# Kernel optimization log

Measured on AMD Instinct MI355X. Metric: run time of the kernel, lower is better.

The kernel has to match this reference:

```python
import jax, jax.numpy as jnp
import numpy as np

B, T, V, D, H, DK = 64, 384, 12, 256, 4, 64

def _ln(x, g, b):
    m = jnp.mean(x, -1, keepdims=True)
    v = jnp.var(x, -1, keepdims=True)
    return (x - m) * jax.lax.rsqrt(v + 1e-5) * g + b

def _grn(x, W1, b1, W2, b2, Wg, bg, lng, lnb, ctx=None, Wc=None, Ws=None, bs=None):
    # eta2 = ELU(fc1(x) + ctx_proj(ctx)); eta1 = fc2(eta2); GLU; residual; LN
    h = x @ W1 + b1
    if ctx is not None:
        h = h + ctx @ Wc
    h = jax.nn.elu(h)
    h = h @ W2 + b2
    g = h @ Wg + bg
    a, gate = jnp.split(g, 2, axis=-1)
    gated = a * jax.nn.sigmoid(gate)
    skip = x if Ws is None else x @ Ws + bs
    return _ln(skip + gated, lng, lnb)

def setup_inputs() -> dict:
    key = jax.random.key(0)
    ks = iter(jax.random.split(key, 48))
    def rn(shape, s=0.02):
        return jax.random.normal(next(ks), shape, jnp.float32) * s
    return {
        'x': jax.random.normal(next(ks), (B, T, V, D), jnp.float32),
        'context': jax.random.normal(next(ks), (B, D), jnp.float32),
        # flattened GRN of VSN: in=V*D, hidden=D, out=V, context=D, skip needed
        'fg_W1': rn((V * D, D)), 'fg_b1': jnp.zeros((D,), jnp.float32),
        'fg_Wc': rn((D, D)),
        'fg_W2': rn((D, D)), 'fg_b2': jnp.zeros((D,), jnp.float32),
        'fg_Wg': rn((D, 2 * V)), 'fg_bg': jnp.zeros((2 * V,), jnp.float32),
        'fg_Ws': rn((V * D, V)), 'fg_bs': jnp.zeros((V,), jnp.float32),
        'fg_lng': jnp.ones((V,), jnp.float32), 'fg_lnb': jnp.zeros((V,), jnp.float32),
        # per-variable GRNs (V of them, in=out=hidden=D, no skip/ctx), stacked
        'sv_W1': rn((V, D, D)), 'sv_b1': jnp.zeros((V, D), jnp.float32),
        'sv_W2': rn((V, D, D)), 'sv_b2': jnp.zeros((V, D), jnp.float32),
        'sv_Wg': rn((V, D, 2 * D)), 'sv_bg': jnp.zeros((V, 2 * D), jnp.float32),
        'sv_lng': jnp.ones((V, D), jnp.float32), 'sv_lnb': jnp.zeros((V, D), jnp.float32),
        # static enrichment GRN: in=out=hidden=D with context
        'en_W1': rn((D, D)), 'en_b1': jnp.zeros((D,), jnp.float32),
        'en_Wc': rn((D, D)),
        'en_W2': rn((D, D)), 'en_b2': jnp.zeros((D,), jnp.float32),
        'en_Wg': rn((D, 2 * D)), 'en_bg': jnp.zeros((2 * D,), jnp.float32),
        'en_lng': jnp.ones((D,), jnp.float32), 'en_lnb': jnp.zeros((D,), jnp.float32),
        # interpretable MHA: per-head Q/K, shared V, output proj
        'Wq': rn((H, D, DK)), 'Wk': rn((H, D, DK)),
        'Wv': rn((D, DK)), 'Wo': rn((DK, D)),
    }

def reference(x, context, fg_W1, fg_b1, fg_Wc, fg_W2, fg_b2, fg_Wg, fg_bg, fg_Ws, fg_bs,
              fg_lng, fg_lnb, sv_W1, sv_b1, sv_W2, sv_b2, sv_Wg, sv_bg, sv_lng, sv_lnb,
              en_W1, en_b1, en_Wc, en_W2, en_b2, en_Wg, en_bg, en_lng, en_lnb,
              Wq, Wk, Wv, Wo):
    b, t, v, d = x.shape
    ctx3 = context[:, None, :]  # broadcast static context over time
    # ---- Variable Selection Network ----
    xf = x.reshape(b, t, v * d)
    w = _grn(xf, fg_W1, fg_b1, fg_W2, fg_b2, fg_Wg, fg_bg, fg_lng, fg_lnb,
             ctx=ctx3, Wc=fg_Wc, Ws=fg_Ws, bs=fg_bs)
    w = jax.nn.softmax(w, axis=-1)  # (b,t,v)
    per_var = jax.vmap(_grn, in_axes=(2, 0, 0, 0, 0, 0, 0, 0, 0), out_axes=2)(
        x, sv_W1, sv_b1, sv_W2, sv_b2, sv_Wg, sv_bg, sv_lng, sv_lnb)  # (b,t,v,d)
    sel = jnp.sum(per_var * w[..., None], axis=2)  # (b,t,d)
    # ---- static enrichment GRN ----
    enr = _grn(sel, en_W1, en_b1, en_W2, en_b2, en_Wg, en_bg, en_lng, en_lnb,
               ctx=ctx3, Wc=en_Wc)
    # ---- interpretable multi-head attention (causal), per-head Q/K, shared V ----
    q = jnp.einsum('btd,hdk->hbtk', enr, Wq)
    k = jnp.einsum('btd,hdk->hbtk', enr, Wk)
    vp = enr @ Wv  # (b,t,dk), shared across heads
    scale = jax.lax.rsqrt(jnp.asarray(DK, jnp.float32))
    scores = jnp.einsum('hbqd,hbkd->hbqk', q, k) * scale
    mask = jnp.triu(jnp.ones((t, t), bool), 1)  # True = masked (future)
    scores = jnp.where(mask, jnp.asarray(-1e9, scores.dtype), scores)
    attn = jax.nn.softmax(scores, axis=-1)
    heads = jnp.einsum('hbqk,bkd->hbqd', attn, vp)
    out = jnp.mean(heads, axis=0) @ Wo  # mean over heads then shared output proj
    return out
```

## Files before the change

kernel.cpp:

```cpp
#include <hip/hip_runtime.h>
#include <hip/hip_bf16.h>
#include <stdint.h>
#include <stddef.h>

typedef __bf16 bf16;
typedef __bf16 bf16x8 __attribute__((ext_vector_type(8)));
typedef float  f32x4  __attribute__((ext_vector_type(4)));

#define BTR 24576
#define EPI_BIAS  1
#define EPI_CVEC  2
#define EPI_ELU   4
#define EPI_ATTN  8
#define EPI_GATE  32
#define EPI_PERM  64

typedef const __attribute__((address_space(1))) void gas_void;
typedef __attribute__((address_space(3))) void sas_void;
__device__ __forceinline__ void gload16(const void* g, void* s) {
  __builtin_amdgcn_global_load_lds((gas_void*)g, (sas_void*)s, 16, 0, 0);
}

__device__ __forceinline__ int perm512(int n) {
  return (n < 256) ? (((n >> 4) << 5) + (n & 15))
                   : ((((n - 256) >> 4) << 5) + ((n - 256) & 15) + 16);
}

template<int EPI, bool AF32, bool CF32>
__global__ __launch_bounds__(256, 2)
void gemm_kernel(const void* __restrict__ Av, int lda, long sAh, long sAb,
                 const bf16* __restrict__ Bt, int ldb, long sBh, long sBb,
                 void* __restrict__ Cv, int ldc, long sC,
                 int K, int zdiv,
                 const float* __restrict__ bias, const float* __restrict__ cvec,
                 long sBias)
{
  __shared__ __align__(16) bf16 As[2][128 * 32];
  __shared__ __align__(16) bf16 Bs[2][128 * 32];

  const int tid  = threadIdx.x;
  const int wave = tid >> 6, lane = tid & 63;
  const int wr = wave >> 1, wc = wave & 1;
  const int quad = lane >> 4, l16 = lane & 15;

  const int z  = blockIdx.z;
  const int hh = z / zdiv, bb = z % zdiv;
  const float* AbF = nullptr; const bf16* AbH = nullptr;
  if constexpr (AF32) AbF = (const float*)Av + (long)hh * sAh + (long)bb * sAb;
  else                AbH = (const bf16*)Av  + (long)hh * sAh + (long)bb * sAb;
  const bf16* Bb = Bt + (long)hh * sBh + (long)bb * sBb;
  float* CbF = nullptr; bf16* CbH = nullptr;
  if constexpr (CF32) CbF = (float*)Cv + (long)z * sC;
  else                CbH = (bf16*)Cv  + (long)z * sC;

  const int rowBase = blockIdx.y * 128;
  const int colBase = blockIdx.x * 128;

  f32x4 acc[4][4];
#pragma unroll
  for (int i = 0; i < 4; ++i)
#pragma unroll
    for (int j = 0; j < 4; ++j) { acc[i][j][0]=0.f; acc[i][j][1]=0.f; acc[i][j][2]=0.f; acc[i][j][3]=0.f; }

  const int r0 = tid >> 2, kc = tid & 3;
  const int r1 = tid >> 1, kh = (tid & 1) * 16;
  const int arow = (wr * 64 + l16) * 32 + quad * 8;
  const int brow = (wc * 64 + l16) * 32 + quad * 8;

  char* AsW = (char*)&As[0][0] + wave * 1024;
  char* BsW = (char*)&Bs[0][0] + wave * 1024;

  f32x4 pf0, pf1, pf2, pf3;
  const int nt = K >> 5;
  int cur = 0;

  if constexpr (AF32) {
    const float* p = AbF + (size_t)(rowBase + r1) * lda + kh;
    pf0 = *(const f32x4*)(p);     pf1 = *(const f32x4*)(p + 4);
    pf2 = *(const f32x4*)(p + 8); pf3 = *(const f32x4*)(p + 12);
  } else {
    gload16(AbH + (size_t)(rowBase + r0)      * lda + kc * 8, AsW);
    gload16(AbH + (size_t)(rowBase + 64 + r0) * lda + kc * 8, AsW + 4096);
  }
  gload16(Bb + (size_t)(colBase + r0)      * ldb + kc * 8, BsW);
  gload16(Bb + (size_t)(colBase + 64 + r0) * ldb + kc * 8, BsW + 4096);
  if constexpr (AF32) {
    bf16x8 a0, a1;
#pragma unroll
    for (int e = 0; e < 4; ++e) {
      a0[e] = (bf16)pf0[e]; a0[4 + e] = (bf16)pf1[e];
      a1[e] = (bf16)pf2[e]; a1[4 + e] = (bf16)pf3[e];
    }
    *(bf16x8*)(&As[0][0] + r1 * 32 + kh)     = a0;
    *(bf16x8*)(&As[0][0] + r1 * 32 + kh + 8) = a1;
  }
  __syncthreads();

  for (int t = 0; t < nt; ++t) {
    const int nxt = cur ^ 1;
    if (t + 1 < nt) {
      const int k1 = (t + 1) * 32;
      if constexpr (AF32) {
        const float* p = AbF + (size_t)(rowBase + r1) * lda + k1 + kh;
        pf0 = *(const f32x4*)(p);     pf1 = *(const f32x4*)(p + 4);
        pf2 = *(const f32x4*)(p + 8); pf3 = *(const f32x4*)(p + 12);
      } else {
        gload16(AbH + (size_t)(rowBase + r0)      * lda + k1 + kc * 8, AsW + nxt * 8192);
        gload16(AbH + (size_t)(rowBase + 64 + r0) * lda + k1 + kc * 8, AsW + nxt * 8192 + 4096);
      }
      gload16(Bb + (size_t)(colBase + r0)      * ldb + k1 + kc * 8, BsW + nxt * 8192);
      gload16(Bb + (size_t)(colBase + 64 + r0) * ldb + k1 + kc * 8, BsW + nxt * 8192 + 4096);
    }

    const bf16* Asc = &As[cur][0];
    const bf16* Bsc = &Bs[cur][0];
    bf16x8 af[4], bfv[4];
#pragma unroll
    for (int mi = 0; mi < 4; ++mi) af[mi]  = *(const bf16x8*)(Asc + arow + mi * 512);
#pragma unroll
    for (int ni = 0; ni < 4; ++ni) bfv[ni] = *(const bf16x8*)(Bsc + brow + ni * 512);
#pragma unroll
    for (int mi = 0; mi < 4; ++mi)
#pragma unroll
      for (int ni = 0; ni < 4; ++ni)
        acc[mi][ni] = __builtin_amdgcn_mfma_f32_16x16x32_bf16(af[mi], bfv[ni], acc[mi][ni], 0, 0, 0);

    if constexpr (AF32) {
      if (t + 1 < nt) {
        bf16x8 a0, a1;
#pragma unroll
        for (int e = 0; e < 4; ++e) {
          a0[e] = (bf16)pf0[e]; a0[4 + e] = (bf16)pf1[e];
          a1[e] = (bf16)pf2[e]; a1[4 + e] = (bf16)pf3[e];
        }
        *(bf16x8*)(&As[nxt][0] + r1 * 32 + kh)     = a0;
        *(bf16x8*)(&As[nxt][0] + r1 * 32 + kh + 8) = a1;
      }
    }
    __syncthreads();
    cur = nxt;
  }

  if constexpr (EPI & EPI_GATE) {
    const float* bp = bias + (size_t)z * sBias;
#pragma unroll
    for (int mi = 0; mi < 4; ++mi) {
#pragma unroll
      for (int nj = 0; nj < 2; ++nj) {
        const int ni = nj * 2;
        const int pa = colBase + wc * 64 + ni * 16 + l16;
        const int j  = (colBase >> 1) + wc * 32 + nj * 16 + l16;
        const float ba = bp[pa], bg = bp[pa + 16];
        const int row0 = rowBase + wr * 64 + mi * 16 + quad * 4;
#pragma unroll
        for (int r = 0; r < 4; ++r) {
          float a = acc[mi][ni][r]     + ba;
          float g = acc[mi][ni + 1][r] + bg;
          CbH[(size_t)(row0 + r) * ldc + j] = (bf16)(a / (1.f + __expf(-g)));
        }
      }
    }
    return;
  }
  const int bctx = (EPI & EPI_CVEC) ? (rowBase / 384) : 0;
  const float* bp = (EPI & EPI_BIAS) ? bias + (size_t)z * sBias : nullptr;
#pragma unroll
  for (int mi = 0; mi < 4; ++mi) {
#pragma unroll
    for (int ni = 0; ni < 4; ++ni) {
      const int row0 = rowBase + wr * 64 + mi * 16 + quad * 4;
      const int col  = colBase + wc * 64 + ni * 16 + l16;
      float bv = (EPI & EPI_BIAS) ? bp[col] : 0.f;
      float cv = (EPI & EPI_CVEC) ? cvec[bctx * 256 + col] : 0.f;
#pragma unroll
      for (int r = 0; r < 4; ++r) {
        float v = acc[mi][ni][r] + bv + cv;
        if (EPI & EPI_ELU)  v = v > 0.f ? v : __expf(v) - 1.f;
        if (EPI & EPI_ATTN) { v *= 0.125f; if (col > row0 + r) v = -1e9f; }
        int srow = row0 + r;
        if constexpr (EPI & EPI_PERM) srow = perm512(srow);
        if constexpr (CF32) CbF[(size_t)srow * ldc + col] = v;
        else                CbH[(size_t)srow * ldc + col] = (bf16)v;
      }
    }
  }
}

__global__ __launch_bounds__(256, 2)
void fgwide_kernel(const float* __restrict__ A, const bf16* __restrict__ Bt,
                   bf16* __restrict__ C, const float* __restrict__ bias,
                   const float* __restrict__ cvec)
{
  __shared__ __align__(16) bf16 As[2][64 * 32];
  __shared__ __align__(16) bf16 Bs[2][384 * 32];
  const int tid = threadIdx.x;
  const int wave = tid >> 6, lane = tid & 63;
  const int quad = lane >> 4, l16 = lane & 15;
  const int rowBase = blockIdx.x * 64;

  f32x4 acc[4][6];
#pragma unroll
  for (int i = 0; i < 4; ++i)
#pragma unroll
    for (int j = 0; j < 6; ++j) { acc[i][j][0]=0.f; acc[i][j][1]=0.f; acc[i][j][2]=0.f; acc[i][j][3]=0.f; }

  const int r1 = tid >> 2, kh = (tid & 3) * 8;
  const int arow = l16 * 32 + quad * 8;
  const int brow = (wave * 96 + l16) * 32 + quad * 8;

  char* BsW = (char*)&Bs[0][0] + wave * 1024;

  f32x4 pf0, pf1;
  int cur = 0;

  {
    const float* p = A + (size_t)(rowBase + r1) * 3072 + kh;
    pf0 = *(const f32x4*)(p); pf1 = *(const f32x4*)(p + 4);
#pragma unroll
    for (int c = 0; c < 6; ++c) {
      const int idx = c * 256 + tid, rb = idx >> 2, kc2 = idx & 3;
      gload16(Bt + (size_t)rb * 3072 + kc2 * 8, BsW + c * 4096);
    }
    bf16x8 av;
#pragma unroll
    for (int e = 0; e < 4; ++e) { av[e] = (bf16)pf0[e]; av[4 + e] = (bf16)pf1[e]; }
    *(bf16x8*)(&As[0][0] + r1 * 32 + kh) = av;
  }
  __syncthreads();

  for (int t = 0; t < 96; ++t) {
    const int nxt = cur ^ 1;
    if (t + 1 < 96) {
      const int k1 = (t + 1) * 32;
      const float* p = A + (size_t)(rowBase + r1) * 3072 + k1 + kh;
      pf0 = *(const f32x4*)(p); pf1 = *(const f32x4*)(p + 4);
#pragma unroll
      for (int c = 0; c < 6; ++c) {
        const int idx = c * 256 + tid, rb = idx >> 2, kc2 = idx & 3;
        gload16(Bt + (size_t)rb * 3072 + k1 + kc2 * 8, BsW + nxt * 24576 + c * 4096);
      }
    }

    const bf16* Asc = &As[cur][0];
    const bf16* Bsc = &Bs[cur][0];
    bf16x8 af[4], bfv[6];
#pragma unroll
    for (int mi = 0; mi < 4; ++mi) af[mi]  = *(const bf16x8*)(Asc + arow + mi * 512);
#pragma unroll
    for (int ni = 0; ni < 6; ++ni) bfv[ni] = *(const bf16x8*)(Bsc + brow + ni * 512);
#pragma unroll
    for (int mi = 0; mi < 4; ++mi)
#pragma unroll
      for (int ni = 0; ni < 6; ++ni)
        acc[mi][ni] = __builtin_amdgcn_mfma_f32_16x16x32_bf16(af[mi], bfv[ni], acc[mi][ni], 0, 0, 0);

    if (t + 1 < 96) {
      bf16x8 av;
#pragma unroll
      for (int e = 0; e < 4; ++e) { av[e] = (bf16)pf0[e]; av[4 + e] = (bf16)pf1[e]; }
      *(bf16x8*)(&As[nxt][0] + r1 * 32 + kh) = av;
    }
    __syncthreads();
    cur = nxt;
  }

  const int bctx = rowBase / 384;
#pragma unroll
  for (int mi = 0; mi < 4; ++mi) {
#pragma unroll
    for (int ni = 0; ni < 6; ++ni) {
      const int col = wave * 96 + ni * 16 + l16;
      const bool act = (wave * 96 + ni * 16) < 256;
      const float bv = bias[col];
      const float cv = act ? cvec[bctx * 256 + col] : 0.f;
      const int row0 = rowBase + mi * 16 + quad * 4;
#pragma unroll
      for (int r = 0; r < 4; ++r) {
        float v = acc[mi][ni][r] + bv + cv;
        if (act) v = v > 0.f ? v : __expf(v) - 1.f;
        C[(size_t)(row0 + r) * 384 + col] = (bf16)v;
      }
    }
  }
}

__global__ void prep_kernel(
    const float* fgW1, const float* fgWs, const float* fgW2, const float* fgWg,
    const float* fgb1, const float* fgbs,
    const float* svW1, const float* svWg, const float* svW2,
    const float* enW1, const float* enWg, const float* enW2,
    const float* Wq, const float* Wk, const float* Wv, const float* Wo,
    bf16* fgW1WsT, bf16* fgWgPT, bf16* fgW2C, float* bias384,
    bf16* svW1T, bf16* svWgT, bf16* svW2C,
    bf16* enW1T, bf16* enWgT, bf16* enW2C,
    bf16* WqkvT, bf16* WoT)
{
  long i = (long)blockIdx.x * 256 + threadIdx.x;
  if (i < 1179648) {
    int n = i / 3072, k = i % 3072; float v;
    if (n < 256) v = fgW1[(size_t)k * 256 + n];
    else { int nn = n - 256; v = (nn < 12) ? fgWs[(size_t)k * 12 + nn] : 0.f; }
    fgW1WsT[i] = (bf16)v; return; } i -= 1179648;
  if (i < 32768)  { int n = i >> 8, k = i & 255; fgWgPT[i] = (n < 24) ? (bf16)fgWg[k * 24 + n] : (bf16)0.f; return; } i -= 32768;
  if (i < 65536)  { fgW2C[i] = (bf16)fgW2[i]; return; } i -= 65536;
  if (i < 384)    { bias384[i] = (i < 256) ? fgb1[i] : ((i < 268) ? fgbs[i - 256] : 0.f); return; } i -= 384;
  if (i < 786432) { long v = i >> 16, r = i & 65535; int n = r >> 8, k = r & 255; svW1T[i] = (bf16)svW1[(v << 16) + k * 256 + n]; return; } i -= 786432;
  if (i < 1572864){ long v = i >> 17, r = i & 131071; int n = r >> 8, k = r & 255; svWgT[i] = (bf16)svWg[(v << 17) + k * 512 + n]; return; } i -= 1572864;
  if (i < 786432) { svW2C[i] = (bf16)svW2[i]; return; } i -= 786432;
  if (i < 65536)  { int n = i >> 8, k = i & 255; enW1T[i] = (bf16)enW1[k * 256 + n]; return; } i -= 65536;
  if (i < 131072) { int n = i >> 8, k = i & 255; enWgT[i] = (bf16)enWg[k * 512 + n]; return; } i -= 131072;
  if (i < 65536)  { enW2C[i] = (bf16)enW2[i]; return; } i -= 65536;
  if (i < 163840) { int n = i >> 8, k = i & 255; float val;
                    if (n < 256)      val = Wq[(n >> 6) * 16384 + k * 64 + (n & 63)];
                    else if (n < 512) { int nn = n - 256; val = Wk[(nn >> 6) * 16384 + k * 64 + (nn & 63)]; }
                    else if (n < 576) val = Wv[k * 64 + (n - 512)];
                    else              val = 0.f;
                    WqkvT[i] = (bf16)val; return; } i -= 163840;
  if (i < 16384)  { int n = i >> 6, k = i & 63; WoT[i] = (bf16)Wo[k * 256 + n]; }
}

__global__ void biasfuse_kernel(const float* fgb2, const float* fgWg, const float* fgbg,
                                const float* svb2, const float* svWg, const float* svbg,
                                const float* enb2, const float* enWg, const float* enbg,
                                float* fgBF, float* svBFP, float* enBFP)
{
  int i = blockIdx.x * 256 + threadIdx.x;
  if (i < 128) {
    float s = 0.f;
    if (i < 24) { s = fgbg[i]; for (int k = 0; k < 256; ++k) s += fgb2[k] * fgWg[k * 24 + i]; }
    fgBF[i] = s; return; } i -= 128;
  if (i < 6144) {
    int v = i >> 9, n = i & 511;
    float s = svbg[v * 512 + n];
    const float* W = svWg + (size_t)v * 131072;
    const float* b2 = svb2 + v * 256;
    for (int k = 0; k < 256; ++k) s += b2[k] * W[k * 512 + n];
    svBFP[v * 512 + perm512(n)] = s; return; } i -= 6144;
  if (i < 512) {
    float s = enbg[i];
    for (int k = 0; k < 256; ++k) s += enb2[k] * enWg[k * 512 + i];
    enBFP[perm512(i)] = s; }
}

__global__ void cvec_kernel(const float* __restrict__ ctx, const float* __restrict__ WcFg,
                            const float* __restrict__ WcEn, float* __restrict__ outFg,
                            float* __restrict__ outEn) {
  int b = blockIdx.x, n = threadIdx.x;
  const float* Wc = blockIdx.y ? WcEn : WcFg;
  float* o = blockIdx.y ? outEn : outFg;
  float acc = 0.f;
  for (int d = 0; d < 256; ++d) acc += ctx[b * 256 + d] * Wc[d * 256 + n];
  o[b * 256 + n] = acc;
}

__global__ void lnsm12_kernel(const bf16* __restrict__ B384, const bf16* __restrict__ GP,
                              const float* __restrict__ lng, const float* __restrict__ lnb,
                              float* __restrict__ w) {
  int r = blockIdx.x * 256 + threadIdx.x;
  if (r >= BTR) return;
  float y[12]; float m = 0.f;
#pragma unroll
  for (int j = 0; j < 12; ++j) {
    float a = (float)GP[(size_t)r * 128 + j];
    float g = (float)GP[(size_t)r * 128 + 12 + j];
    float gated = a / (1.f + __expf(-g));
    y[j] = (float)B384[(size_t)r * 384 + 256 + j] + gated; m += y[j];
  }
  m *= (1.f / 12.f);
  float var = 0.f;
#pragma unroll
  for (int j = 0; j < 12; ++j) { float d = y[j] - m; var += d * d; }
  var *= (1.f / 12.f);
  float rstd = rsqrtf(var + 1e-5f);
  float mx = -1e30f;
#pragma unroll
  for (int j = 0; j < 12; ++j) { y[j] = (y[j] - m) * rstd * lng[j] + lnb[j]; mx = fmaxf(mx, y[j]); }
  float s = 0.f;
#pragma unroll
  for (int j = 0; j < 12; ++j) { y[j] = __expf(y[j] - mx); s += y[j]; }
  float inv = 1.f / s;
#pragma unroll
  for (int j = 0; j < 12; ++j) w[r * 12 + j] = y[j] * inv;
}

__device__ __forceinline__ void block_sum2(float a, float b, float& oa, float& ob) {
#pragma unroll
  for (int o = 32; o; o >>= 1) { a += __shfl_xor(a, o); b += __shfl_xor(b, o); }
  __shared__ float ra[4], rb[4];
  int w = threadIdx.x >> 6;
  if ((threadIdx.x & 63) == 0) { ra[w] = a; rb[w] = b; }
  __syncthreads();
  oa = ra[0] + ra[1] + ra[2] + ra[3];
  ob = rb[0] + rb[1] + rb[2] + rb[3];
  __syncthreads();
}

__global__ __launch_bounds__(256)
void selacc4_kernel(const bf16* __restrict__ GATED, const float* __restrict__ x,
                    const float* __restrict__ w, const float* __restrict__ lng,
                    const float* __restrict__ lnb, float* __restrict__ sel,
                    bf16* __restrict__ selb, int v0, int isFirst, int isLast) {
  int r = blockIdx.x, d = threadIdx.x;
  float acc = isFirst ? 0.f : sel[(size_t)r * 256 + d];
#pragma unroll
  for (int vv = 0; vv < 4; ++vv) {
    int v = v0 + vv;
    float gated = (float)GATED[(size_t)vv * ((size_t)BTR * 256) + (size_t)r * 256 + d];
    float y = x[(size_t)r * 3072 + v * 256 + d] + gated;
    float s1, s2;
    block_sum2(y, y * y, s1, s2);
    float mean = s1 * (1.f / 256.f);
    float var  = s2 * (1.f / 256.f) - mean * mean;
    float val  = (y - mean) * rsqrtf(var + 1e-5f) * lng[v * 256 + d] + lnb[v * 256 + d];
    acc += w[r * 12 + v] * val;
  }
  if (isLast) selb[(size_t)r * 256 + d] = (bf16)acc;
  else        sel[(size_t)r * 256 + d] = acc;
}

__global__ __launch_bounds__(256)
void enrln_kernel(const bf16* __restrict__ GATED, const bf16* __restrict__ skip,
                  const float* __restrict__ lng, const float* __restrict__ lnb,
                  bf16* __restrict__ out) {
  int r = blockIdx.x, d = threadIdx.x;
  float gated = (float)GATED[(size_t)r * 256 + d];
  float y = (float)skip[(size_t)r * 256 + d] + gated;
  float s1, s2;
  block_sum2(y, y * y, s1, s2);
  float mean = s1 * (1.f / 256.f);
  float var = s2 * (1.f / 256.f) - mean * mean;
  float norm = (y - mean) * rsqrtf(var + 1e-5f);
  out[(size_t)r * 256 + d] = (bf16)(norm * lng[d] + lnb[d]);
}

__global__ __launch_bounds__(384)
void softmax_avg_kernel(const bf16* __restrict__ S, bf16* __restrict__ P) {
  const int bq = blockIdx.x;
  const int b = bq / 384, q = bq % 384;
  const int j = threadIdx.x;
  const int w = j >> 6;
  __shared__ float red[6];
  float pb = 0.f;
  for (int h = 0; h < 4; ++h) {
    float s = (float)S[((size_t)((h * 64 + b) * 384 + q)) * 384 + j];
    float m = s;
#pragma unroll
    for (int o = 32; o; o >>= 1) m = fmaxf(m, __shfl_xor(m, o));
    if ((j & 63) == 0) red[w] = m;
    __syncthreads();
    m = fmaxf(fmaxf(fmaxf(red[0], red[1]), fmaxf(red[2], red[3])), fmaxf(red[4], red[5]));
    __syncthreads();
    float e = __expf(s - m);
    float l = e;
#pragma unroll
    for (int o = 32; o; o >>= 1) l += __shfl_xor(l, o);
    if ((j & 63) == 0) red[w] = l;
    __syncthreads();
    l = red[0] + red[1] + red[2] + red[3] + red[4] + red[5];
    __syncthreads();
    pb += e / l;
  }
  P[(size_t)bq * 384 + j] = (bf16)(0.25f * pb);
}

template<int EPI, bool AF32, bool CF32>
static inline void rungemm(hipStream_t s,
    const void* A, int lda, const bf16* Bt, int ldb, void* C, int ldc,
    int M, int N, int K,
    const float* bias = nullptr, const float* cvec = nullptr,
    int Z = 1, int zdiv = 1,
    long sAh = 0, long sAb = 0, long sBh = 0, long sBb = 0, long sC = 0, long sBias = 0)
{
  dim3 grid(N / 128, M / 128, Z);
  gemm_kernel<EPI, AF32, CF32><<<grid, 256, 0, s>>>(A, lda, sAh, sAb, Bt, ldb, sBh, sBb, C, ldc, sC, K, zdiv, bias, cvec, sBias);
}

extern "C" void kernel_launch(void* const* d_in, const int* in_sizes, int n_in,
                              void* d_out, int out_size, void* d_ws, size_t ws_size,
                              hipStream_t stream)
{
  (void)in_sizes; (void)n_in; (void)out_size;
  const float* x      = (const float*)d_in[0];
  const float* ctx    = (const float*)d_in[1];
  const float* fg_W1  = (const float*)d_in[2];
  const float* fg_b1  = (const float*)d_in[3];
  const float* fg_Wc  = (const float*)d_in[4];
  const float* fg_W2  = (const float*)d_in[5];
  const float* fg_b2  = (const float*)d_in[6];
  const float* fg_Wg  = (const float*)d_in[7];
  const float* fg_bg  = (const float*)d_in[8];
  const float* fg_Ws  = (const float*)d_in[9];
  const float* fg_bs  = (const float*)d_in[10];
  const float* fg_lng = (const float*)d_in[11];
  const float* fg_lnb = (const float*)d_in[12];
  const float* sv_W1  = (const float*)d_in[13];
  const float* sv_b1  = (const float*)d_in[14];
  const float* sv_W2  = (const float*)d_in[15];
  const float* sv_b2  = (const float*)d_in[16];
  const float* sv_Wg  = (const float*)d_in[17];
  const float* sv_bg  = (const float*)d_in[18];
  const float* sv_lng = (const float*)d_in[19];
  const float* sv_lnb = (const float*)d_in[20];
  const float* en_W1  = (const float*)d_in[21];
  const float* en_b1  = (const float*)d_in[22];
  const float* en_Wc  = (const float*)d_in[23];
  const float* en_W2  = (const float*)d_in[24];
  const float* en_b2  = (const float*)d_in[25];
  const float* en_Wg  = (const float*)d_in[26];
  const float* en_bg  = (const float*)d_in[27];
  const float* en_lng = (const float*)d_in[28];
  const float* en_lnb = (const float*)d_in[29];
  const float* Wq     = (const float*)d_in[30];
  const float* Wk     = (const float*)d_in[31];
  const float* Wv     = (const float*)d_in[32];
  const float* Wo     = (const float*)d_in[33];

  static constexpr size_t OFF_FGW1WST = 0;
  static constexpr size_t OFF_FGWGPT  = OFF_FGW1WST + 2359296;
  static constexpr size_t OFF_FGW2C   = OFF_FGWGPT  + 65536;
  static constexpr size_t OFF_FGW2GT  = OFF_FGW2C   + 131072;
  static constexpr size_t OFF_BIAS384 = OFF_FGW2GT  + 65536;
  static constexpr size_t OFF_FGBF    = OFF_BIAS384 + 1536;
  static constexpr size_t OFF_SVW1T   = OFF_FGBF    + 512;
  static constexpr size_t OFF_SVWGT   = OFF_SVW1T   + 1572864;
  static constexpr size_t OFF_SVW2C   = OFF_SVWGT   + 3145728;
  static constexpr size_t OFF_SVW2GPT = OFF_SVW2C   + 1572864;
  static constexpr size_t OFF_SVBFP   = OFF_SVW2GPT + 3145728;
  static constexpr size_t OFF_ENW1T   = OFF_SVBFP   + 24576;
  static constexpr size_t OFF_ENWGT   = OFF_ENW1T   + 131072;
  static constexpr size_t OFF_ENW2C   = OFF_ENWGT   + 262144;
  static constexpr size_t OFF_ENW2GPT = OFF_ENW2C   + 131072;
  static constexpr size_t OFF_ENBFP   = OFF_ENW2GPT + 262144;
  static constexpr size_t OFF_WQKVT   = OFF_ENBFP   + 2048;
  static constexpr size_t OFF_WOT     = OFF_WQKVT   + 327680;
  static constexpr size_t OFF_CVECFG  = OFF_WOT     + 32768;
  static constexpr size_t OFF_CVECEN  = OFF_CVECFG  + 65536;
  static constexpr size_t ARENA       = OFF_CVECEN  + 65536;
  static constexpr size_t WS_NEEDED = ARENA + 152174592;

  if (ws_size < WS_NEEDED) return;

  char* ws = (char*)d_ws;
  bf16*  fgW1WsT = (bf16*)(ws + OFF_FGW1WST);
  bf16*  fgWgPT  = (bf16*)(ws + OFF_FGWGPT);
  bf16*  fgW2C   = (bf16*)(ws + OFF_FGW2C);
  bf16*  fgW2gT  = (bf16*)(ws + OFF_FGW2GT);
  float* bias384 = (float*)(ws + OFF_BIAS384);
  float* fgBF    = (float*)(ws + OFF_FGBF);
  bf16*  svW1T   = (bf16*)(ws + OFF_SVW1T);
  bf16*  svWgT   = (bf16*)(ws + OFF_SVWGT);
  bf16*  svW2C   = (bf16*)(ws + OFF_SVW2C);
  bf16*  svW2gPT = (bf16*)(ws + OFF_SVW2GPT);
  float* svBFP   = (float*)(ws + OFF_SVBFP);
  bf16*  enW1T   = (bf16*)(ws + OFF_ENW1T);
  bf16*  enWgT   = (bf16*)(ws + OFF_ENWGT);
  bf16*  enW2C   = (bf16*)(ws + OFF_ENW2C);
  bf16*  enW2gPT = (bf16*)(ws + OFF_ENW2GPT);
  float* enBFP   = (float*)(ws + OFF_ENBFP);
  bf16*  WqkvT   = (bf16*)(ws + OFF_WQKVT);
  bf16*  WoT     = (bf16*)(ws + OFF_WOT);
  float* cvecFg  = (float*)(ws + OFF_CVECFG);
  float* cvecEn  = (float*)(ws + OFF_CVECEN);
  char*  ar      = ws + ARENA;
  float* sel     = (float*)(ar + 0);
  bf16*  selb    = (bf16*)(ar + 25165824);
  float* wbuf    = (float*)(ar + 37748736);
  bf16*  H1G     = (bf16*)(ar + 38928384);
  bf16*  BUF384  = (bf16*)(ar + 38928384);
  bf16*  GPAD    = (bf16*)(ar + 57802752);
  bf16*  H1EN    = (bf16*)(ar + 38928384);
  bf16*  GATED   = (bf16*)(ar + 89260032);
  bf16*  GATEDEN = (bf16*)(ar + 89260032);
  bf16*  enr     = (bf16*)(ar + 139591680);
  bf16*  QKV     = (bf16*)(ar + 0);
  bf16*  Pbar    = (bf16*)(ar + 38928384);
  bf16*  Sbuf    = (bf16*)(ar + 64094208);
  bf16*  UT      = (bf16*)(ar + 64094208);
  float* out     = (float*)d_out;

  prep_kernel<<<19010, 256, 0, stream>>>(fg_W1, fg_Ws, fg_W2, fg_Wg, fg_b1, fg_bs,
                                         sv_W1, sv_Wg, sv_W2, en_W1, en_Wg, en_W2,
                                         Wq, Wk, Wv, Wo,
                                         fgW1WsT, fgWgPT, fgW2C, bias384,
                                         svW1T, svWgT, svW2C, enW1T, enWgT, enW2C,
                                         WqkvT, WoT);
  biasfuse_kernel<<<27, 256, 0, stream>>>(fg_b2, fg_Wg, fg_bg, sv_b2, sv_Wg, sv_bg,
                                          en_b2, en_Wg, en_bg, fgBF, svBFP, enBFP);
  cvec_kernel<<<dim3(64, 2), 256, 0, stream>>>(ctx, fg_Wc, en_Wc, cvecFg, cvecEn);

  rungemm<0,        false, false>(stream, fgWgPT, 256, fgW2C, 256, fgW2gT, 256, 128, 256, 256);
  rungemm<EPI_PERM, false, false>(stream, svWgT, 256, svW2C, 256, svW2gPT, 256, 512, 256, 256,
                                  nullptr, nullptr, 12, 12, 0, 131072, 0, 65536, 131072);
  rungemm<EPI_PERM, false, false>(stream, enWgT, 256, enW2C, 256, enW2gPT, 256, 512, 256, 256);

  fgwide_kernel<<<384, 256, 0, stream>>>(x, fgW1WsT, BUF384, bias384, cvecFg);
  rungemm<EPI_BIAS, false, false>(stream, BUF384, 384, fgW2gT, 256, GPAD, 128, BTR, 128, 256, fgBF);
  lnsm12_kernel<<<96, 256, 0, stream>>>(BUF384, GPAD, fg_lng, fg_lnb, wbuf);

  for (int g = 0; g < 3; ++g) {
    rungemm<EPI_BIAS|EPI_ELU, true, false>(
        stream, x + g * 4 * 256, 3072, svW1T + (size_t)g * 4 * 65536, 256, H1G, 256, BTR, 256, 256,
        sv_b1 + g * 4 * 256, nullptr, 4, 4, 0, 256, 0, 65536, (long)BTR * 256, 256);
    rungemm<EPI_BIAS|EPI_GATE, false, false>(
        stream, H1G, 256, svW2gPT + (size_t)g * 4 * 131072, 256, GATED, 256, BTR, 512, 256,
        svBFP + g * 4 * 512, nullptr, 4, 4, 0, (long)BTR * 256, 0, 131072, (long)BTR * 256, 512);
    selacc4_kernel<<<BTR, 256, 0, stream>>>(GATED, x, wbuf, sv_lng, sv_lnb, sel, selb,
                                            g * 4, g == 0, g == 2);
  }

  rungemm<EPI_BIAS|EPI_CVEC|EPI_ELU, false, false>(stream, selb, 256, enW1T, 256, H1EN, 256, BTR, 256, 256, en_b1, cvecEn);
  rungemm<EPI_BIAS|EPI_GATE, false, false>(stream, H1EN, 256, enW2gPT, 256, GATEDEN, 256, BTR, 512, 256, enBFP);
  enrln_kernel<<<BTR, 256, 0, stream>>>(GATEDEN, selb, en_lng, en_lnb, enr);

  rungemm<0, false, false>(stream, enr, 256, WqkvT, 256, QKV, 640, BTR, 640, 256);
  rungemm<EPI_ATTN, false, false>(stream, QKV, 640, QKV + 256, 640, Sbuf, 384, 384, 384, 64,
                                  nullptr, nullptr, 256, 64, 64, 245760L, 64, 245760L, 147456L);
  softmax_avg_kernel<<<BTR, 384, 0, stream>>>(Sbuf, Pbar);
  rungemm<0, false, false>(stream, WoT, 64, QKV + 512, 640, UT, 384, 256, 384, 64,
                           nullptr, nullptr, 64, 64, 0, 0, 0, 245760L, 98304L);
  rungemm<0, false, true>(stream, Pbar, 384, UT, 384, out, 256, 384, 256, 384,
                          nullptr, nullptr, 64, 1, 147456L, 0, 98304L, 0, 98304L);
}
```

Measured before the change: 1.361 ms.

## Load full K into LDS up front for small-K GEMMs; wave-per-row softmax

Adds a compile-time KT path to the GEMM that issues every K-tile's global-to-LDS load at once and then consumes the tiles in order using vmcnt waits and barriers, instead of the double-buffered loop. It is enabled for all bf16-A GEMMs with K of 256 or 64. This removes the per-tile load/compute serialization and loop sync overhead. The cost is more LDS (64KB per block at K=256), which can lower occupancy below the two blocks per CU the launch bounds target. Softmax is also rewritten so each wave handles one row with shuffles only, removing the LDS reductions and block barriers.

```diff
diff --git a/kernel.cpp b/kernel.cpp
--- a/kernel.cpp
+++ b/kernel.cpp
@@ -20,13 +20,16 @@
 __device__ __forceinline__ void gload16(const void* g, void* s) {
   __builtin_amdgcn_global_load_lds((gas_void*)g, (sas_void*)s, 16, 0, 0);
 }
+template<int N> __device__ __forceinline__ void waitvm() {
+  asm volatile("s_waitcnt vmcnt(%0)" :: "n"(N) : "memory");
+}
 
 __device__ __forceinline__ int perm512(int n) {
   return (n < 256) ? (((n >> 4) << 5) + (n & 15))
                    : ((((n - 256) >> 4) << 5) + ((n - 256) & 15) + 16);
 }
 
-template<int EPI, bool AF32, bool CF32>
+template<int EPI, bool AF32, bool CF32, int KT = 0>
 __global__ __launch_bounds__(256, 2)
 void gemm_kernel(const void* __restrict__ Av, int lda, long sAh, long sAb,
                  const bf16* __restrict__ Bt, int ldb, long sBh, long sBb,
@@ -35,8 +38,9 @@
                  const float* __restrict__ bias, const float* __restrict__ cvec,
                  long sBias)
 {
-  __shared__ __align__(16) bf16 As[2][128 * 32];
-  __shared__ __align__(16) bf16 Bs[2][128 * 32];
+  constexpr int NBUF = (KT > 0) ? (KT / 32) : 2;
+  __shared__ __align__(16) bf16 As[NBUF][128 * 32];
+  __shared__ __align__(16) bf16 Bs[NBUF][128 * 32];
 
   const int tid  = threadIdx.x;
   const int wave = tid >> 6, lane = tid & 63;
@@ -67,78 +71,111 @@
   const int arow = (wr * 64 + l16) * 32 + quad * 8;
   const int brow = (wc * 64 + l16) * 32 + quad * 8;
 
-  char* AsW = (char*)&As[0][0] + wave * 1024;
-  char* BsW = (char*)&Bs[0][0] + wave * 1024;
-
-  f32x4 pf0, pf1, pf2, pf3;
-  const int nt = K >> 5;
-  int cur = 0;
-
-  if constexpr (AF32) {
-    const float* p = AbF + (size_t)(rowBase + r1) * lda + kh;
-    pf0 = *(const f32x4*)(p);     pf1 = *(const f32x4*)(p + 4);
-    pf2 = *(const f32x4*)(p + 8); pf3 = *(const f32x4*)(p + 12);
+  if constexpr (KT > 0) {
+    constexpr int NT = KT / 32;
+    char* AsB = (char*)&As[0][0] + wave * 1024;
+    char* BsB = (char*)&Bs[0][0] + wave * 1024;
+#pragma unroll
+    for (int t = 0; t < NT; ++t) {
+      const int k0 = t * 32;
+      gload16(AbH + (size_t)(rowBase + r0)      * lda + k0 + kc * 8, AsB + t * 8192);
+      gload16(AbH + (size_t)(rowBase + 64 + r0) * lda + k0 + kc * 8, AsB + t * 8192 + 4096);
+      gload16(Bb  + (size_t)(colBase + r0)      * ldb + k0 + kc * 8, BsB + t * 8192);
+      gload16(Bb  + (size_t)(colBase + 64 + r0) * ldb + k0 + kc * 8, BsB + t * 8192 + 4096);
+    }
+#define FP_TILE(T)                                                                 \
+    if constexpr ((T) < NT) {                                                      \
+      waitvm<(NT - 1 - (T)) * 4>();                                                \
+      __builtin_amdgcn_s_barrier();                                                \
+      const bf16* Asc = &As[(T)][0];                                               \
+      const bf16* Bsc = &Bs[(T)][0];                                               \
+      bf16x8 af[4], bfv[4];                                                        \
+      _Pragma("unroll")                                                            \
+      for (int mi = 0; mi < 4; ++mi) af[mi]  = *(const bf16x8*)(Asc + arow + mi * 512); \
+      _Pragma("unroll")                                                            \
+      for (int ni = 0; ni < 4; ++ni) bfv[ni] = *(const bf16x8*)(Bsc + brow + ni * 512); \
+      _Pragma("unroll")                                                            \
+      for (int mi = 0; mi < 4; ++mi)                                               \
+        _Pragma("unroll")                                                          \
+        for (int ni = 0; ni < 4; ++ni)                                             \
+          acc[mi][ni] = __builtin_amdgcn_mfma_f32_16x16x32_bf16(af[mi], bfv[ni], acc[mi][ni], 0, 0, 0); \
+    }
+    FP_TILE(0) FP_TILE(1) FP_TILE(2) FP_TILE(3)
+    FP_TILE(4) FP_TILE(5) FP_TILE(6) FP_TILE(7)
+#undef FP_TILE
   } else {
-    gload16(AbH + (size_t)(rowBase + r0)      * lda + kc * 8, AsW);
-    gload16(AbH + (size_t)(rowBase + 64 + r0) * lda + kc * 8, AsW + 4096);
-  }
-  gload16(Bb + (size_t)(colBase + r0)      * ldb + kc * 8, BsW);
-  gload16(Bb + (size_t)(colBase + 64 + r0) * ldb + kc * 8, BsW + 4096);
-  if constexpr (AF32) {
-    bf16x8 a0, a1;
-#pragma unroll
-    for (int e = 0; e < 4; ++e) {
-      a0[e] = (bf16)pf0[e]; a0[4 + e] = (bf16)pf1[e];
-      a1[e] = (bf16)pf2[e]; a1[4 + e] = (bf16)pf3[e];
-    }
-    *(bf16x8*)(&As[0][0] + r1 * 32 + kh)     = a0;
-    *(bf16x8*)(&As[0][0] + r1 * 32 + kh + 8) = a1;
-  }
-  __syncthreads();
-
-  for (int t = 0; t < nt; ++t) {
-    const int nxt = cur ^ 1;
-    if (t + 1 < nt) {
-      const int k1 = (t + 1) * 32;
+    char* AsW = (char*)&As[0][0] + wave * 1024;
+    char* BsW = (char*)&Bs[0][0] + wave * 1024;
+    f32x4 pf0, pf1, pf2, pf3;
+    const int nt = K >> 5;
+    int cur = 0;
+
+    if constexpr (AF32) {
+      const float* p = AbF + (size_t)(rowBase + r1) * lda + kh;
+      pf0 = *(const f32x4*)(p);     pf1 = *(const f32x4*)(p + 4);
+      pf2 = *(const f32x4*)(p + 8); pf3 = *(const f32x4*)(p + 12);
+    } else {
+      gload16(AbH + (size_t)(rowBase + r0)      * lda + kc * 8, AsW);
+      gload16(AbH + (size_t)(rowBase + 64 + r0) * lda + kc * 8, AsW + 4096);
+    }
+    gload16(Bb + (size_t)(colBase + r0)      * ldb + kc * 8, BsW);
+    gload16(Bb + (size_t)(colBase + 64 + r0) * ldb + kc * 8, BsW + 4096);
+    if constexpr (AF32) {
+      bf16x8 a0, a1;
+#pragma unroll
+      for (int e = 0; e < 4; ++e) {
+        a0[e] = (bf16)pf0[e]; a0[4 + e] = (bf16)pf1[e];
+        a1[e] = (bf16)pf2[e]; a1[4 + e] = (bf16)pf3[e];
+      }
+      *(bf16x8*)(&As[0][0] + r1 * 32 + kh)     = a0;
+      *(bf16x8*)(&As[0][0] + r1 * 32 + kh + 8) = a1;
+    }
+    __syncthreads();
+
+    for (int t = 0; t < nt; ++t) {
+      const int nxt = cur ^ 1;
+      if (t + 1 < nt) {
+        const int k1 = (t + 1) * 32;
+        if constexpr (AF32) {
+          const float* p = AbF + (size_t)(rowBase + r1) * lda + k1 + kh;
+          pf0 = *(const f32x4*)(p);     pf1 = *(const f32x4*)(p + 4);
+          pf2 = *(const f32x4*)(p + 8); pf3 = *(const f32x4*)(p + 12);
+        } else {
+          gload16(AbH + (size_t)(rowBase + r0)      * lda + k1 + kc * 8, AsW + nxt * 8192);
+          gload16(AbH + (size_t)(rowBase + 64 + r0) * lda + k1 + kc * 8, AsW + nxt * 8192 + 4096);
+        }
+        gload16(Bb + (size_t)(colBase + r0)      * ldb + k1 + kc * 8, BsW + nxt * 8192);
+        gload16(Bb + (size_t)(colBase + 64 + r0) * ldb + k1 + kc * 8, BsW + nxt * 8192 + 4096);
+      }
+
+      const bf16* Asc = &As[cur][0];
+      const bf16* Bsc = &Bs[cur][0];
+      bf16x8 af[4], bfv[4];
+#pragma unroll
+      for (int mi = 0; mi < 4; ++mi) af[mi]  = *(const bf16x8*)(Asc + arow + mi * 512);
+#pragma unroll
+      for (int ni = 0; ni < 4; ++ni) bfv[ni] = *(const bf16x8*)(Bsc + brow + ni * 512);
+#pragma unroll
+      for (int mi = 0; mi < 4; ++mi)
+#pragma unroll
+        for (int ni = 0; ni < 4; ++ni)
+          acc[mi][ni] = __builtin_amdgcn_mfma_f32_16x16x32_bf16(af[mi], bfv[ni], acc[mi][ni], 0, 0, 0);
+
       if constexpr (AF32) {
-        const float* p = AbF + (size_t)(rowBase + r1) * lda + k1 + kh;
-        pf0 = *(const f32x4*)(p);     pf1 = *(const f32x4*)(p + 4);
-        pf2 = *(const f32x4*)(p + 8); pf3 = *(const f32x4*)(p + 12);
-      } else {
-        gload16(AbH + (size_t)(rowBase + r0)      * lda + k1 + kc * 8, AsW + nxt * 8192);
-        gload16(AbH + (size_t)(rowBase + 64 + r0) * lda + k1 + kc * 8, AsW + nxt * 8192 + 4096);
+        if (t + 1 < nt) {
+          bf16x8 a0, a1;
+#pragma unroll
+          for (int e = 0; e < 4; ++e) {
+            a0[e] = (bf16)pf0[e]; a0[4 + e] = (bf16)pf1[e];
+            a1[e] = (bf16)pf2[e]; a1[4 + e] = (bf16)pf3[e];
+          }
+          *(bf16x8*)(&As[nxt][0] + r1 * 32 + kh)     = a0;
+          *(bf16x8*)(&As[nxt][0] + r1 * 32 + kh + 8) = a1;
+        }
       }
-      gload16(Bb + (size_t)(colBase + r0)      * ldb + k1 + kc * 8, BsW + nxt * 8192);
-      gload16(Bb + (size_t)(colBase + 64 + r0) * ldb + k1 + kc * 8, BsW + nxt * 8192 + 4096);
-    }
-
-    const bf16* Asc = &As[cur][0];
-    const bf16* Bsc = &Bs[cur][0];
-    bf16x8 af[4], bfv[4];
-#pragma unroll
-    for (int mi = 0; mi < 4; ++mi) af[mi]  = *(const bf16x8*)(Asc + arow + mi * 512);
-#pragma unroll
-    for (int ni = 0; ni < 4; ++ni) bfv[ni] = *(const bf16x8*)(Bsc + brow + ni * 512);
-#pragma unroll
-    for (int mi = 0; mi < 4; ++mi)
-#pragma unroll
-      for (int ni = 0; ni < 4; ++ni)
-        acc[mi][ni] = __builtin_amdgcn_mfma_f32_16x16x32_bf16(af[mi], bfv[ni], acc[mi][ni], 0, 0, 0);
-
-    if constexpr (AF32) {
-      if (t + 1 < nt) {
-        bf16x8 a0, a1;
-#pragma unroll
-        for (int e = 0; e < 4; ++e) {
-          a0[e] = (bf16)pf0[e]; a0[4 + e] = (bf16)pf1[e];
-          a1[e] = (bf16)pf2[e]; a1[4 + e] = (bf16)pf3[e];
-        }
-        *(bf16x8*)(&As[nxt][0] + r1 * 32 + kh)     = a0;
-        *(bf16x8*)(&As[nxt][0] + r1 * 32 + kh + 8) = a1;
-      }
-    }
-    __syncthreads();
-    cur = nxt;
+      __syncthreads();
+      cur = nxt;
+    }
   }
 
   if constexpr (EPI & EPI_GATE) {
@@ -433,37 +470,36 @@
   out[(size_t)r * 256 + d] = (bf16)(norm * lng[d] + lnb[d]);
 }
 
-__global__ __launch_bounds__(384)
+__global__ __launch_bounds__(256)
 void softmax_avg_kernel(const bf16* __restrict__ S, bf16* __restrict__ P) {
-  const int bq = blockIdx.x;
+  const int wv = threadIdx.x >> 6, lane = threadIdx.x & 63;
+  const int bq = blockIdx.x * 4 + wv;
   const int b = bq / 384, q = bq % 384;
-  const int j = threadIdx.x;
-  const int w = j >> 6;
-  __shared__ float red[6];
-  float pb = 0.f;
+  float pb[6];
+#pragma unroll
+  for (int e = 0; e < 6; ++e) pb[e] = 0.f;
   for (int h = 0; h < 4; ++h) {
-    float s = (float)S[((size_t)((h * 64 + b) * 384 + q)) * 384 + j];
-    float m = s;
+    const bf16* row = S + ((size_t)((h * 64 + b) * 384 + q)) * 384;
+    float v[6]; float m = -1e30f;
+#pragma unroll
+    for (int e = 0; e < 6; ++e) { v[e] = (float)row[lane + e * 64]; m = fmaxf(m, v[e]); }
 #pragma unroll
     for (int o = 32; o; o >>= 1) m = fmaxf(m, __shfl_xor(m, o));
-    if ((j & 63) == 0) red[w] = m;
-    __syncthreads();
-    m = fmaxf(fmaxf(fmaxf(red[0], red[1]), fmaxf(red[2], red[3])), fmaxf(red[4], red[5]));
-    __syncthreads();
-    float e = __expf(s - m);
-    float l = e;
+    float l = 0.f;
+#pragma unroll
+    for (int e = 0; e < 6; ++e) { v[e] = __expf(v[e] - m); l += v[e]; }
 #pragma unroll
     for (int o = 32; o; o >>= 1) l += __shfl_xor(l, o);
-    if ((j & 63) == 0) red[w] = l;
-    __syncthreads();
-    l = red[0] + red[1] + red[2] + red[3] + red[4] + red[5];
-    __syncthreads();
-    pb += e / l;
-  }
-  P[(size_t)bq * 384 + j] = (bf16)(0.25f * pb);
-}
-
-template<int EPI, bool AF32, bool CF32>
+    float inv = 1.f / l;
+#pragma unroll
+    for (int e = 0; e < 6; ++e) pb[e] += v[e] * inv;
+  }
+  bf16* out = P + (size_t)bq * 384;
+#pragma unroll
+  for (int e = 0; e < 6; ++e) out[lane + e * 64] = (bf16)(0.25f * pb[e]);
+}
+
+template<int EPI, bool AF32, bool CF32, int KT = 0>
 static inline void rungemm(hipStream_t s,
     const void* A, int lda, const bf16* Bt, int ldb, void* C, int ldc,
     int M, int N, int K,
@@ -472,7 +508,7 @@
     long sAh = 0, long sAb = 0, long sBh = 0, long sBb = 0, long sC = 0, long sBias = 0)
 {
   dim3 grid(N / 128, M / 128, Z);
-  gemm_kernel<EPI, AF32, CF32><<<grid, 256, 0, s>>>(A, lda, sAh, sAb, Bt, ldb, sBh, sBb, C, ldc, sC, K, zdiv, bias, cvec, sBias);
+  gemm_kernel<EPI, AF32, CF32, KT><<<grid, 256, 0, s>>>(A, lda, sAh, sAb, Bt, ldb, sBh, sBb, C, ldc, sC, K, zdiv, bias, cvec, sBias);
 }
 
 extern "C" void kernel_launch(void* const* d_in, const int* in_sizes, int n_in,
@@ -588,36 +624,36 @@
                                           en_b2, en_Wg, en_bg, fgBF, svBFP, enBFP);
   cvec_kernel<<<dim3(64, 2), 256, 0, stream>>>(ctx, fg_Wc, en_Wc, cvecFg, cvecEn);
 
-  rungemm<0,        false, false>(stream, fgWgPT, 256, fgW2C, 256, fgW2gT, 256, 128, 256, 256);
-  rungemm<EPI_PERM, false, false>(stream, svWgT, 256, svW2C, 256, svW2gPT, 256, 512, 256, 256,
-                                  nullptr, nullptr, 12, 12, 0, 131072, 0, 65536, 131072);
-  rungemm<EPI_PERM, false, false>(stream, enWgT, 256, enW2C, 256, enW2gPT, 256, 512, 256, 256);
+  rungemm<0,        false, false, 256>(stream, fgWgPT, 256, fgW2C, 256, fgW2gT, 256, 128, 256, 256);
+  rungemm<EPI_PERM, false, false, 256>(stream, svWgT, 256, svW2C, 256, svW2gPT, 256, 512, 256, 256,
+                                       nullptr, nullptr, 12, 12, 0, 131072, 0, 65536, 131072);
+  rungemm<EPI_PERM, false, false, 256>(stream, enWgT, 256, enW2C, 256, enW2gPT, 256, 512, 256, 256);
 
   fgwide_kernel<<<384, 256, 0, stream>>>(x, fgW1WsT, BUF384, bias384, cvecFg);
-  rungemm<EPI_BIAS, false, false>(stream, BUF384, 384, fgW2gT, 256, GPAD, 128, BTR, 128, 256, fgBF);
+  rungemm<EPI_BIAS, false, false, 256>(stream, BUF384, 384, fgW2gT, 256, GPAD, 128, BTR, 128, 256, fgBF);
   lnsm12_kernel<<<96, 256, 0, stream>>>(BUF384, GPAD, fg_lng, fg_lnb, wbuf);
 
   for (int g = 0; g < 3; ++g) {
     rungemm<EPI_BIAS|EPI_ELU, true, false>(
         stream, x + g * 4 * 256, 3072, svW1T + (size_t)g * 4 * 65536, 256, H1G, 256, BTR, 256, 256,
         sv_b1 + g * 4 * 256, nullptr, 4, 4, 0, 256, 0, 65536, (long)BTR * 256, 256);
-    rungemm<EPI_BIAS|EPI_GATE, false, false>(
+    rungemm<EPI_BIAS|EPI_GATE, false, false, 256>(
         stream, H1G, 256, svW2gPT + (size_t)g * 4 * 131072, 256, GATED, 256, BTR, 512, 256,
         svBFP + g * 4 * 512, nullptr, 4, 4, 0, (long)BTR * 256, 0, 131072, (long)BTR * 256, 512);
     selacc4_kernel<<<BTR, 256, 0, stream>>>(GATED, x, wbuf, sv_lng, sv_lnb, sel, selb,
                                             g * 4, g == 0, g == 2);
   }
 
-  rungemm<EPI_BIAS|EPI_CVEC|EPI_ELU, false, false>(stream, selb, 256, enW1T, 256, H1EN, 256, BTR, 256, 256, en_b1, cvecEn);
-  rungemm<EPI_BIAS|EPI_GATE, false, false>(stream, H1EN, 256, enW2gPT, 256, GATEDEN, 256, BTR, 512, 256, enBFP);
+  rungemm<EPI_BIAS|EPI_CVEC|EPI_ELU, false, false, 256>(stream, selb, 256, enW1T, 256, H1EN, 256, BTR, 256, 256, en_b1, cvecEn);
+  rungemm<EPI_BIAS|EPI_GATE, false, false, 256>(stream, H1EN, 256, enW2gPT, 256, GATEDEN, 256, BTR, 512, 256, enBFP);
   enrln_kernel<<<BTR, 256, 0, stream>>>(GATEDEN, selb, en_lng, en_lnb, enr);
 
-  rungemm<0, false, false>(stream, enr, 256, WqkvT, 256, QKV, 640, BTR, 640, 256);
-  rungemm<EPI_ATTN, false, false>(stream, QKV, 640, QKV + 256, 640, Sbuf, 384, 384, 384, 64,
-                                  nullptr, nullptr, 256, 64, 64, 245760L, 64, 245760L, 147456L);
-  softmax_avg_kernel<<<BTR, 384, 0, stream>>>(Sbuf, Pbar);
-  rungemm<0, false, false>(stream, WoT, 64, QKV + 512, 640, UT, 384, 256, 384, 64,
-                           nullptr, nullptr, 64, 64, 0, 0, 0, 245760L, 98304L);
+  rungemm<0, false, false, 256>(stream, enr, 256, WqkvT, 256, QKV, 640, BTR, 640, 256);
+  rungemm<EPI_ATTN, false, false, 64>(stream, QKV, 640, QKV + 256, 640, Sbuf, 384, 384, 384, 64,
+                                      nullptr, nullptr, 256, 64, 64, 245760L, 64, 245760L, 147456L);
+  softmax_avg_kernel<<<6144, 256, 0, stream>>>(Sbuf, Pbar);
+  rungemm<0, false, false, 64>(stream, WoT, 64, QKV + 512, 640, UT, 384, 256, 384, 64,
+                               nullptr, nullptr, 64, 64, 0, 0, 0, 245760L, 98304L);
   rungemm<0, false, true>(stream, Pbar, 384, UT, 384, out, 256, 384, 256, 384,
                           nullptr, nullptr, 64, 1, 147456L, 0, 98304L, 0, 98304L);
 }
```

Result: no change. 1.369 ms (+0.5%).
